# Kernel optimization log

Hardware: AMD Instinct MI355X
Metric: run time of the kernel (lower is better)

The kernel has to match this reference:

```python
import jax, jax.numpy as jnp
import numpy as np

REGION = 64  # region_size r

def setup_inputs() -> dict:
    key = jax.random.key(0)
    B, C, H, W, k, r, T = 16, 64, 256, 256, 3, REGION, 32
    k0, k1, k2, k3, k4 = jax.random.split(key, 5)
    x = jax.random.normal(k0, (B, C, H, W), dtype=jnp.float32)
    weight = jax.random.normal(k1, (C, C, k, k), dtype=jnp.float32) * 0.05  # [out,in,kh,kw]
    h_idx = jax.random.randint(k2, (T,), 0, H - r + 1, dtype=jnp.int32)
    w_idx = jax.random.randint(k3, (T,), 0, W - r + 1, dtype=jnp.int32)
    lambdas = jax.random.uniform(k4, (T,), dtype=jnp.float32)
    return {"x": x, "weight": weight, "h_idx": h_idx, "w_idx": w_idx, "lambdas": lambdas}

def reference(x, weight, h_idx, w_idx, lambdas):
    B, C, H, W = x.shape
    k = weight.shape[-1]
    r = REGION
    n_r = (H // r) * (W // r)
    out_r = r - k + 1  # conv 'VALID' output size per region

    def step(out, t):
        h, w, lam = t
        crop = jax.lax.dynamic_slice(x, (0, 0, h, w), (B, C, r, r))
        c = jax.lax.conv_general_dilated(
            crop, weight, window_strides=(1, 1), padding='VALID',
            dimension_numbers=('NCHW', 'OIHW', 'NCHW'))
        cur = jax.lax.dynamic_slice(out, (0, 0, h, w), (B, C, out_r, out_r))
        out = jax.lax.dynamic_update_slice(out, cur + lam * c, (0, 0, h, w))
        return out, None

    out, _ = jax.lax.scan(step, jnp.zeros_like(x), (h_idx, w_idx, lambdas))
    return out / n_r
```

## Files before the change

kernel.cpp:

```cpp
#include <hip/hip_runtime.h>


typedef short short8 __attribute__((ext_vector_type(8)));
typedef float floatx4 __attribute__((ext_vector_type(4)));
typedef unsigned int uint4v __attribute__((ext_vector_type(4)));

#define OUTR 62

__device__ inline unsigned f2bf_pack(float lo, float hi) {
    unsigned ul = __builtin_bit_cast(unsigned, lo);
    unsigned uh = __builtin_bit_cast(unsigned, hi);
    ul = (ul + 0x7FFFu + ((ul >> 16) & 1u)) >> 16;
    uh = (uh + 0x7FFFu + ((uh >> 16) & 1u)) >> 16;
    return ul | (uh << 16);
}

__global__ void srconv_coeff_kernel(const int* __restrict__ h_idx,
                                    const int* __restrict__ w_idx,
                                    const float* __restrict__ lam,
                                    int T, float* __restrict__ coeff) {
    int p = blockIdx.x;
    int q = threadIdx.x;
    float c = 0.f;
    for (int t = 0; t < T; ++t) {
        int dh = p - h_idx[t];
        int dw = q - w_idx[t];
        if (dh >= 0 && dh < OUTR && dw >= 0 && dw < OUTR) c += lam[t];
    }
    coeff[(p << 8) + q] = c * (1.0f / 16.0f);
}

__global__ void srconv_wtrans_kernel(const float* __restrict__ wgt,
                                     uint4v* __restrict__ afrag) {
    int id = blockIdx.x * 256 + threadIdx.x;
    int l  = id & 63;
    int fi = id >> 6;
    int m  = fi & 3;
    int cb = (fi >> 2) & 1;
    int kk = fi >> 3;
    int co  = m * 16 + (l & 15);
    int ci0 = cb * 32 + (l >> 4) * 8;
    float w[8];
#pragma unroll
    for (int j = 0; j < 8; ++j)
        w[j] = wgt[(co * 64 + ci0 + j) * 9 + kk];
    uint4v d;
    d.x = f2bf_pack(w[0], w[1]);
    d.y = f2bf_pack(w[2], w[3]);
    d.z = f2bf_pack(w[4], w[5]);
    d.w = f2bf_pack(w[6], w[7]);
    afrag[id] = d;
}

__launch_bounds__(256, 2)
__global__ void srconv_fused_kernel(const float* __restrict__ x,
                                    const float* __restrict__ coeff,
                                    const uint4v* __restrict__ afrag,
                                    float* __restrict__ out) {
    __shared__ __align__(16) unsigned xs[2 * 340 * 16];
    __shared__ __align__(16) uint4v af_lds[2304];

    const int tid  = threadIdx.x;
    const int lane = tid & 63;
    const int wv   = tid >> 6;
    const int l15  = lane & 15;
    const int kg   = lane >> 4;

    const unsigned bid = blockIdx.x;
    const unsigned swz = (bid & 7) * 512 + (bid >> 3);
    const int b    = swz >> 8;
    const int tile = swz & 255;
    const int P0   = (tile >> 3) << 3;
    const int Q0   = (tile & 7) << 5;

    float myc = coeff[((P0 + (tid >> 5)) << 8) + Q0 + (tid & 31)];
    if (__syncthreads_count(myc != 0.f) == 0) {
        const floatx4 z = (floatx4){0.f, 0.f, 0.f, 0.f};
        for (int u = tid; u < 64 * 8 * 8; u += 256) {
            int q4 = u & 7;
            int pr = (u >> 3) & 7;
            int co = u >> 6;
            *(floatx4*)(out + (((b << 6) + co) << 16) +
                        ((P0 + pr) << 8) + Q0 + (q4 << 2)) = z;
        }
        return;
    }

    const int prb = P0 + (wv << 1);

    float cf[2][2];
#pragma unroll
    for (int p = 0; p < 2; ++p)
#pragma unroll
        for (int h = 0; h < 2; ++h)
            cf[p][h] = coeff[((prb + p) << 8) + Q0 + (h << 4) + l15];

    const float* xb = x + ((size_t)b << 22);

    floatx4 va[6][2], vb[6][2];
    uint4v  vc[9];

#pragma unroll
    for (int i = 0; i < 9; ++i) {
        int e = i * 256 + tid;
        vc[i] = afrag[e + ((e >> 8) << 8)];
    }
#pragma unroll
    for (int r = 0; r < 6; ++r) {
        int u  = r * 256 + tid;
        int uc = u < 1440 ? u : 1439;
        int cp    = uc / 90;
        int rem   = uc - cp * 90;
        int row   = rem / 9;
        int chunk = rem - row * 9;
        int gr    = min(P0 + row, 255);
        int gcb   = min(Q0 + (chunk << 2), 252);
        const float* xp = xb + (cp << 17) + (gr << 8) + gcb;
        va[r][0] = *(const floatx4*)(xp);
        va[r][1] = *(const floatx4*)(xp + 65536);
    }

#pragma unroll
    for (int i = 0; i < 9; ++i)
        af_lds[i * 256 + tid] = vc[i];
#pragma unroll
    for (int r = 0; r < 6; ++r) {
        int u  = r * 256 + tid;
        int uc = u < 1440 ? u : 1439;
        int cp    = uc / 90;
        int rem   = uc - cp * 90;
        int row   = rem / 9;
        int chunk = rem - row * 9;
        int c4 = chunk << 2;
#pragma unroll
        for (int j = 0; j < 4; ++j) {
            if (u < 1440 && c4 + j < 34) {
                int pix = row * 34 + c4 + j;
                int slot = cp ^ (((pix >> 1) & 3) << 2);
                xs[(pix << 4) + slot] = f2bf_pack(va[r][0][j], va[r][1][j]);
            }
        }
    }

#pragma unroll
    for (int r = 0; r < 6; ++r) {
        int u  = r * 256 + tid;
        int uc = u < 1440 ? u : 1439;
        int cp    = uc / 90;
        int rem   = uc - cp * 90;
        int row   = rem / 9;
        int chunk = rem - row * 9;
        int gr    = min(P0 + row, 255);
        int gcb   = min(Q0 + (chunk << 2), 252);
        const float* xp = xb + ((16 + cp) << 17) + (gr << 8) + gcb;
        vb[r][0] = *(const floatx4*)(xp);
        vb[r][1] = *(const floatx4*)(xp + 65536);
    }
#pragma unroll
    for (int i = 0; i < 9; ++i) {
        int e = i * 256 + tid;
        vc[i] = afrag[e + ((e >> 8) << 8) + 256];
    }
    __syncthreads();

    floatx4 acc[4][2][2];
#pragma unroll
    for (int m = 0; m < 4; ++m)
#pragma unroll
        for (int p = 0; p < 2; ++p)
#pragma unroll
            for (int h = 0; h < 2; ++h)
                acc[m][p][h] = (floatx4){0.f, 0.f, 0.f, 0.f};

#pragma unroll 2
    for (int t = 0; t < 9; ++t) {
        const int kh = t / 3;
        const int kw = t - kh * 3;

        short8 a[4];
#pragma unroll
        for (int m = 0; m < 4; ++m)
            a[m] = *reinterpret_cast<const short8*>(
                &af_lds[(t << 8) + (m << 6) + lane]);
        short8 bf[2][2];
#pragma unroll
        for (int p = 0; p < 2; ++p)
#pragma unroll
            for (int h = 0; h < 2; ++h) {
                int prl = (wv << 1) + p + kh;
                int cl  = (h << 4) + l15 + kw;
                int pix = prl * 34 + cl;
                int off = (pix << 4) +
                          ((kg << 2) ^ (((pix >> 1) & 3) << 2));
                bf[p][h] = *(const short8*)(&xs[off]);
            }
        __builtin_amdgcn_s_setprio(1);
#pragma unroll
        for (int m = 0; m < 4; ++m)
#pragma unroll
            for (int p = 0; p < 2; ++p)
#pragma unroll
                for (int h = 0; h < 2; ++h)
                    acc[m][p][h] = __builtin_amdgcn_mfma_f32_16x16x32_bf16(
                        a[m], bf[p][h], acc[m][p][h], 0, 0, 0);
        __builtin_amdgcn_s_setprio(0);
    }
    __syncthreads();

#pragma unroll
    for (int r = 0; r < 6; ++r) {
        int u  = r * 256 + tid;
        int uc = u < 1440 ? u : 1439;
        int cp    = uc / 90;
        int rem   = uc - cp * 90;
        int row   = rem / 9;
        int chunk = rem - row * 9;
        int c4 = chunk << 2;
#pragma unroll
        for (int j = 0; j < 4; ++j) {
            if (u < 1440 && c4 + j < 34) {
                int pix = row * 34 + c4 + j;
                int slot = cp ^ (((pix >> 1) & 3) << 2);
                xs[5440 + (pix << 4) + slot] =
                    f2bf_pack(vb[r][0][j], vb[r][1][j]);
            }
        }
    }
#pragma unroll
    for (int i = 0; i < 9; ++i)
        af_lds[i * 256 + tid] = vc[i];
    __syncthreads();

#pragma unroll 2
    for (int t = 0; t < 9; ++t) {
        const int kh = t / 3;
        const int kw = t - kh * 3;

        short8 a[4];
#pragma unroll
        for (int m = 0; m < 4; ++m)
            a[m] = *reinterpret_cast<const short8*>(
                &af_lds[(t << 8) + (m << 6) + lane]);
        short8 bf[2][2];
#pragma unroll
        for (int p = 0; p < 2; ++p)
#pragma unroll
            for (int h = 0; h < 2; ++h) {
                int prl = (wv << 1) + p + kh;
                int cl  = (h << 4) + l15 + kw;
                int pix = prl * 34 + cl;
                int off = 5440 + (pix << 4) +
                          ((kg << 2) ^ (((pix >> 1) & 3) << 2));
                bf[p][h] = *(const short8*)(&xs[off]);
            }
        __builtin_amdgcn_s_setprio(1);
#pragma unroll
        for (int m = 0; m < 4; ++m)
#pragma unroll
            for (int p = 0; p < 2; ++p)
#pragma unroll
                for (int h = 0; h < 2; ++h)
                    acc[m][p][h] = __builtin_amdgcn_mfma_f32_16x16x32_bf16(
                        a[m], bf[p][h], acc[m][p][h], 0, 0, 0);
        __builtin_amdgcn_s_setprio(0);
    }
    __syncthreads();

    float* epb = reinterpret_cast<float*>(xs);
    const int co_l = lane >> 3;
    const int q4   = lane & 7;

#pragma unroll
    for (int p = 0; p < 2; ++p) {
        const int pr = prb + p;
#pragma unroll
        for (int m = 0; m < 4; ++m) {
            float* ep = epb + (((wv << 1) + (m & 1)) * 576);
#pragma unroll
            for (int h = 0; h < 2; ++h)
#pragma unroll
                for (int reg = 0; reg < 4; ++reg)
                    ep[((kg << 2) + reg) * 36 + (h << 4) + l15] =
                        acc[m][p][h][reg] * cf[p][h];
#pragma unroll
            for (int j = 0; j < 2; ++j) {
                const floatx4 v = *reinterpret_cast<const floatx4*>(
                    &ep[(co_l + (j << 3)) * 36 + (q4 << 2)]);
                const int co = (m << 4) + co_l + (j << 3);
                *(floatx4*)(out + (((b << 6) + co) << 16) +
                            (pr << 8) + Q0 + (q4 << 2)) = v;
            }
        }
    }
}

extern "C" void kernel_launch(void* const* d_in, const int* in_sizes, int n_in,
                              void* d_out, int out_size, void* d_ws, size_t ws_size,
                              hipStream_t stream) {
    const float* x     = (const float*)d_in[0];
    const float* wgt   = (const float*)d_in[1];
    const int*   h_idx = (const int*)d_in[2];
    const int*   w_idx = (const int*)d_in[3];
    const float* lam   = (const float*)d_in[4];
    float*       out   = (float*)d_out;
    float*       coeff = (float*)d_ws;
    char*        af_b  = (char*)d_ws + 65536 * sizeof(float);
    const int    T     = in_sizes[2];

    srconv_coeff_kernel<<<256, 256, 0, stream>>>(h_idx, w_idx, lam, T, coeff);
    srconv_wtrans_kernel<<<18, 256, 0, stream>>>(wgt, (uint4v*)af_b);
    srconv_fused_kernel<<<4096, 256, 0, stream>>>(
        x, coeff, (const uint4v*)af_b, out);
}
```

Baseline: 169.8 us.

## Process two row-tiles per block with cross-tile prefetch of inputs and weights

Each block now covers 16 output rows as two 8-row sub-tiles, and the grid is halved. Global loads for the next sub-tile's input channels and weight fragments are issued while the current sub-tile is still computing and storing. The epilogue staging moves to the second LDS half so the first half can be refilled early. This aims to hide load latency and amortize per-block setup, at the cost of more register pressure, coarser zero-tile skipping and fewer blocks available for load balancing.

```diff
diff --git a/kernel.cpp b/kernel.cpp
--- a/kernel.cpp
+++ b/kernel.cpp
@@ -67,231 +67,228 @@
     const int kg   = lane >> 4;
 
     const unsigned bid = blockIdx.x;
-    const unsigned swz = (bid & 7) * 512 + (bid >> 3);
-    const int b    = swz >> 8;
-    const int tile = swz & 255;
-    const int P0   = (tile >> 3) << 3;
-    const int Q0   = (tile & 7) << 5;
-
-    float myc = coeff[((P0 + (tid >> 5)) << 8) + Q0 + (tid & 31)];
-    if (__syncthreads_count(myc != 0.f) == 0) {
+    const unsigned swz = (bid & 7) * 256 + (bid >> 3);
+    const int b    = swz >> 7;
+    const int rest = swz & 127;
+    const int R0   = (rest >> 3) << 4;
+    const int Q0   = (rest & 7) << 5;
+
+    float cm = 0.f;
+#pragma unroll
+    for (int i = 0; i < 2; ++i) {
+        int u = i * 256 + tid;
+        cm = fmaxf(cm, coeff[((R0 + (u >> 5)) << 8) + Q0 + (u & 31)]);
+    }
+    if (__syncthreads_count(cm != 0.f) == 0) {
         const floatx4 z = (floatx4){0.f, 0.f, 0.f, 0.f};
-        for (int u = tid; u < 64 * 8 * 8; u += 256) {
+        for (int u = tid; u < 64 * 16 * 8; u += 256) {
             int q4 = u & 7;
-            int pr = (u >> 3) & 7;
-            int co = u >> 6;
+            int pr = (u >> 3) & 15;
+            int co = u >> 7;
             *(floatx4*)(out + (((b << 6) + co) << 16) +
-                        ((P0 + pr) << 8) + Q0 + (q4 << 2)) = z;
+                        ((R0 + pr) << 8) + Q0 + (q4 << 2)) = z;
         }
         return;
     }
-
-    const int prb = P0 + (wv << 1);
-
-    float cf[2][2];
-#pragma unroll
-    for (int p = 0; p < 2; ++p)
-#pragma unroll
-        for (int h = 0; h < 2; ++h)
-            cf[p][h] = coeff[((prb + p) << 8) + Q0 + (h << 4) + l15];
 
     const float* xb = x + ((size_t)b << 22);
 
     floatx4 va[6][2], vb[6][2];
     uint4v  vc[9];
 
-#pragma unroll
-    for (int i = 0; i < 9; ++i) {
-        int e = i * 256 + tid;
-        vc[i] = afrag[e + ((e >> 8) << 8)];
-    }
-#pragma unroll
-    for (int r = 0; r < 6; ++r) {
-        int u  = r * 256 + tid;
-        int uc = u < 1440 ? u : 1439;
-        int cp    = uc / 90;
-        int rem   = uc - cp * 90;
-        int row   = rem / 9;
-        int chunk = rem - row * 9;
-        int gr    = min(P0 + row, 255);
-        int gcb   = min(Q0 + (chunk << 2), 252);
-        const float* xp = xb + (cp << 17) + (gr << 8) + gcb;
-        va[r][0] = *(const floatx4*)(xp);
-        va[r][1] = *(const floatx4*)(xp + 65536);
-    }
-
-#pragma unroll
-    for (int i = 0; i < 9; ++i)
-        af_lds[i * 256 + tid] = vc[i];
-#pragma unroll
-    for (int r = 0; r < 6; ++r) {
-        int u  = r * 256 + tid;
-        int uc = u < 1440 ? u : 1439;
-        int cp    = uc / 90;
-        int rem   = uc - cp * 90;
-        int row   = rem / 9;
-        int chunk = rem - row * 9;
-        int c4 = chunk << 2;
-#pragma unroll
-        for (int j = 0; j < 4; ++j) {
-            if (u < 1440 && c4 + j < 34) {
-                int pix = row * 34 + c4 + j;
-                int slot = cp ^ (((pix >> 1) & 3) << 2);
-                xs[(pix << 4) + slot] = f2bf_pack(va[r][0][j], va[r][1][j]);
-            }
-        }
-    }
-
-#pragma unroll
-    for (int r = 0; r < 6; ++r) {
-        int u  = r * 256 + tid;
-        int uc = u < 1440 ? u : 1439;
-        int cp    = uc / 90;
-        int rem   = uc - cp * 90;
-        int row   = rem / 9;
-        int chunk = rem - row * 9;
-        int gr    = min(P0 + row, 255);
-        int gcb   = min(Q0 + (chunk << 2), 252);
-        const float* xp = xb + ((16 + cp) << 17) + (gr << 8) + gcb;
-        vb[r][0] = *(const floatx4*)(xp);
-        vb[r][1] = *(const floatx4*)(xp + 65536);
-    }
-#pragma unroll
-    for (int i = 0; i < 9; ++i) {
-        int e = i * 256 + tid;
-        vc[i] = afrag[e + ((e >> 8) << 8) + 256];
-    }
+#define ISSUE_A(CB)                                                         \
+    _Pragma("unroll")                                                       \
+    for (int i_ = 0; i_ < 9; ++i_) {                                        \
+        int e_ = i_ * 256 + tid;                                            \
+        vc[i_] = afrag[e_ + ((e_ >> 8) << 8) + ((CB) << 8)];                \
+    }
+#define WRITE_A()                                                           \
+    _Pragma("unroll")                                                       \
+    for (int i_ = 0; i_ < 9; ++i_) af_lds[i_ * 256 + tid] = vc[i_];
+#define ISSUE_X(P0N, CB, V)                                                 \
+    _Pragma("unroll")                                                       \
+    for (int r_ = 0; r_ < 6; ++r_) {                                        \
+        int u_  = r_ * 256 + tid;                                           \
+        int uc_ = u_ < 1440 ? u_ : 1439;                                    \
+        int cp_    = uc_ / 90;                                              \
+        int rem_   = uc_ - cp_ * 90;                                        \
+        int row_   = rem_ / 9;                                              \
+        int chunk_ = rem_ - row_ * 9;                                       \
+        int gr_    = min((P0N) + row_, 255);                                \
+        int gcb_   = min(Q0 + (chunk_ << 2), 252);                          \
+        const float* xp_ = xb + ((((CB) << 4) + cp_) << 17) +               \
+                           (gr_ << 8) + gcb_;                               \
+        V[r_][0] = *(const floatx4*)(xp_);                                  \
+        V[r_][1] = *(const floatx4*)(xp_ + 65536);                          \
+    }
+#define WRITE_X(OFF, V)                                                     \
+    _Pragma("unroll")                                                       \
+    for (int r_ = 0; r_ < 6; ++r_) {                                        \
+        int u_  = r_ * 256 + tid;                                           \
+        int uc_ = u_ < 1440 ? u_ : 1439;                                    \
+        int cp_    = uc_ / 90;                                              \
+        int rem_   = uc_ - cp_ * 90;                                        \
+        int row_   = rem_ / 9;                                              \
+        int chunk_ = rem_ - row_ * 9;                                       \
+        int c4_ = chunk_ << 2;                                              \
+        _Pragma("unroll")                                                   \
+        for (int j_ = 0; j_ < 4; ++j_) {                                    \
+            if (u_ < 1440 && c4_ + j_ < 34) {                               \
+                int pix_  = row_ * 34 + c4_ + j_;                           \
+                int slot_ = cp_ ^ (((pix_ >> 1) & 3) << 2);                 \
+                xs[(OFF) + (pix_ << 4) + slot_] =                           \
+                    f2bf_pack(V[r_][0][j_], V[r_][1][j_]);                  \
+            }                                                               \
+        }                                                                   \
+    }
+
+    ISSUE_A(0);
+    ISSUE_X(R0, 0, va);
+    WRITE_A();
+    WRITE_X(0, va);
+    ISSUE_X(R0, 1, vb);
+    ISSUE_A(1);
     __syncthreads();
 
-    floatx4 acc[4][2][2];
-#pragma unroll
-    for (int m = 0; m < 4; ++m)
-#pragma unroll
-        for (int p = 0; p < 2; ++p)
-#pragma unroll
-            for (int h = 0; h < 2; ++h)
-                acc[m][p][h] = (floatx4){0.f, 0.f, 0.f, 0.f};
-
-#pragma unroll 2
-    for (int t = 0; t < 9; ++t) {
-        const int kh = t / 3;
-        const int kw = t - kh * 3;
-
-        short8 a[4];
-#pragma unroll
-        for (int m = 0; m < 4; ++m)
-            a[m] = *reinterpret_cast<const short8*>(
-                &af_lds[(t << 8) + (m << 6) + lane]);
-        short8 bf[2][2];
-#pragma unroll
-        for (int p = 0; p < 2; ++p)
-#pragma unroll
-            for (int h = 0; h < 2; ++h) {
-                int prl = (wv << 1) + p + kh;
-                int cl  = (h << 4) + l15 + kw;
-                int pix = prl * 34 + cl;
-                int off = (pix << 4) +
-                          ((kg << 2) ^ (((pix >> 1) & 3) << 2));
-                bf[p][h] = *(const short8*)(&xs[off]);
-            }
-        __builtin_amdgcn_s_setprio(1);
-#pragma unroll
-        for (int m = 0; m < 4; ++m)
-#pragma unroll
-            for (int p = 0; p < 2; ++p)
-#pragma unroll
-                for (int h = 0; h < 2; ++h)
-                    acc[m][p][h] = __builtin_amdgcn_mfma_f32_16x16x32_bf16(
-                        a[m], bf[p][h], acc[m][p][h], 0, 0, 0);
-        __builtin_amdgcn_s_setprio(0);
-    }
-    __syncthreads();
-
-#pragma unroll
-    for (int r = 0; r < 6; ++r) {
-        int u  = r * 256 + tid;
-        int uc = u < 1440 ? u : 1439;
-        int cp    = uc / 90;
-        int rem   = uc - cp * 90;
-        int row   = rem / 9;
-        int chunk = rem - row * 9;
-        int c4 = chunk << 2;
-#pragma unroll
-        for (int j = 0; j < 4; ++j) {
-            if (u < 1440 && c4 + j < 34) {
-                int pix = row * 34 + c4 + j;
-                int slot = cp ^ (((pix >> 1) & 3) << 2);
-                xs[5440 + (pix << 4) + slot] =
-                    f2bf_pack(vb[r][0][j], vb[r][1][j]);
-            }
-        }
-    }
-#pragma unroll
-    for (int i = 0; i < 9; ++i)
-        af_lds[i * 256 + tid] = vc[i];
-    __syncthreads();
-
-#pragma unroll 2
-    for (int t = 0; t < 9; ++t) {
-        const int kh = t / 3;
-        const int kw = t - kh * 3;
-
-        short8 a[4];
-#pragma unroll
-        for (int m = 0; m < 4; ++m)
-            a[m] = *reinterpret_cast<const short8*>(
-                &af_lds[(t << 8) + (m << 6) + lane]);
-        short8 bf[2][2];
-#pragma unroll
-        for (int p = 0; p < 2; ++p)
-#pragma unroll
-            for (int h = 0; h < 2; ++h) {
-                int prl = (wv << 1) + p + kh;
-                int cl  = (h << 4) + l15 + kw;
-                int pix = prl * 34 + cl;
-                int off = 5440 + (pix << 4) +
-                          ((kg << 2) ^ (((pix >> 1) & 3) << 2));
-                bf[p][h] = *(const short8*)(&xs[off]);
-            }
-        __builtin_amdgcn_s_setprio(1);
-#pragma unroll
-        for (int m = 0; m < 4; ++m)
-#pragma unroll
-            for (int p = 0; p < 2; ++p)
-#pragma unroll
-                for (int h = 0; h < 2; ++h)
-                    acc[m][p][h] = __builtin_amdgcn_mfma_f32_16x16x32_bf16(
-                        a[m], bf[p][h], acc[m][p][h], 0, 0, 0);
-        __builtin_amdgcn_s_setprio(0);
-    }
-    __syncthreads();
-
-    float* epb = reinterpret_cast<float*>(xs);
     const int co_l = lane >> 3;
     const int q4   = lane & 7;
 
 #pragma unroll
-    for (int p = 0; p < 2; ++p) {
-        const int pr = prb + p;
-#pragma unroll
-        for (int m = 0; m < 4; ++m) {
-            float* ep = epb + (((wv << 1) + (m & 1)) * 576);
+    for (int s = 0; s < 2; ++s) {
+        const int P0  = R0 + (s << 3);
+        const int prb = P0 + (wv << 1);
+
+        float cf[2][2];
+#pragma unroll
+        for (int p = 0; p < 2; ++p)
 #pragma unroll
             for (int h = 0; h < 2; ++h)
-#pragma unroll
-                for (int reg = 0; reg < 4; ++reg)
-                    ep[((kg << 2) + reg) * 36 + (h << 4) + l15] =
-                        acc[m][p][h][reg] * cf[p][h];
-#pragma unroll
-            for (int j = 0; j < 2; ++j) {
-                const floatx4 v = *reinterpret_cast<const floatx4*>(
-                    &ep[(co_l + (j << 3)) * 36 + (q4 << 2)]);
-                const int co = (m << 4) + co_l + (j << 3);
-                *(floatx4*)(out + (((b << 6) + co) << 16) +
-                            (pr << 8) + Q0 + (q4 << 2)) = v;
+                cf[p][h] = coeff[((prb + p) << 8) + Q0 + (h << 4) + l15];
+
+        floatx4 acc[4][2][2];
+#pragma unroll
+        for (int m = 0; m < 4; ++m)
+#pragma unroll
+            for (int p = 0; p < 2; ++p)
+#pragma unroll
+                for (int h = 0; h < 2; ++h)
+                    acc[m][p][h] = (floatx4){0.f, 0.f, 0.f, 0.f};
+
+#pragma unroll 2
+        for (int t = 0; t < 9; ++t) {
+            const int kh = t / 3;
+            const int kw = t - kh * 3;
+            short8 a[4];
+#pragma unroll
+            for (int m = 0; m < 4; ++m)
+                a[m] = *reinterpret_cast<const short8*>(
+                    &af_lds[(t << 8) + (m << 6) + lane]);
+            short8 bf[2][2];
+#pragma unroll
+            for (int p = 0; p < 2; ++p)
+#pragma unroll
+                for (int h = 0; h < 2; ++h) {
+                    int prl = (wv << 1) + p + kh;
+                    int cl  = (h << 4) + l15 + kw;
+                    int pix = prl * 34 + cl;
+                    int off = (pix << 4) +
+                              ((kg << 2) ^ (((pix >> 1) & 3) << 2));
+                    bf[p][h] = *(const short8*)(&xs[off]);
+                }
+            __builtin_amdgcn_s_setprio(1);
+#pragma unroll
+            for (int m = 0; m < 4; ++m)
+#pragma unroll
+                for (int p = 0; p < 2; ++p)
+#pragma unroll
+                    for (int h = 0; h < 2; ++h)
+                        acc[m][p][h] = __builtin_amdgcn_mfma_f32_16x16x32_bf16(
+                            a[m], bf[p][h], acc[m][p][h], 0, 0, 0);
+            __builtin_amdgcn_s_setprio(0);
+        }
+        __syncthreads();
+
+        WRITE_X(5440, vb);
+        WRITE_A();
+        if (s == 0) {
+            ISSUE_X(R0 + 8, 0, va);
+            ISSUE_A(0);
+        }
+        __syncthreads();
+
+#pragma unroll 2
+        for (int t = 0; t < 9; ++t) {
+            const int kh = t / 3;
+            const int kw = t - kh * 3;
+            short8 a[4];
+#pragma unroll
+            for (int m = 0; m < 4; ++m)
+                a[m] = *reinterpret_cast<const short8*>(
+                    &af_lds[(t << 8) + (m << 6) + lane]);
+            short8 bf[2][2];
+#pragma unroll
+            for (int p = 0; p < 2; ++p)
+#pragma unroll
+                for (int h = 0; h < 2; ++h) {
+                    int prl = (wv << 1) + p + kh;
+                    int cl  = (h << 4) + l15 + kw;
+                    int pix = prl * 34 + cl;
+                    int off = 5440 + (pix << 4) +
+                              ((kg << 2) ^ (((pix >> 1) & 3) << 2));
+                    bf[p][h] = *(const short8*)(&xs[off]);
+                }
+            __builtin_amdgcn_s_setprio(1);
+#pragma unroll
+            for (int m = 0; m < 4; ++m)
+#pragma unroll
+                for (int p = 0; p < 2; ++p)
+#pragma unroll
+                    for (int h = 0; h < 2; ++h)
+                        acc[m][p][h] = __builtin_amdgcn_mfma_f32_16x16x32_bf16(
+                            a[m], bf[p][h], acc[m][p][h], 0, 0, 0);
+            __builtin_amdgcn_s_setprio(0);
+        }
+        __syncthreads();
+
+        if (s == 0) {
+            WRITE_X(0, va);
+            WRITE_A();
+        }
+
+        float* epb = reinterpret_cast<float*>(xs) + 5440;
+#pragma unroll
+        for (int p = 0; p < 2; ++p) {
+            const int pr = prb + p;
+#pragma unroll
+            for (int m = 0; m < 4; ++m) {
+                float* ep = epb + (((wv << 1) + (m & 1)) * 576);
+#pragma unroll
+                for (int h = 0; h < 2; ++h)
+#pragma unroll
+                    for (int reg = 0; reg < 4; ++reg)
+                        ep[((kg << 2) + reg) * 36 + (h << 4) + l15] =
+                            acc[m][p][h][reg] * cf[p][h];
+#pragma unroll
+                for (int j = 0; j < 2; ++j) {
+                    const floatx4 v = *reinterpret_cast<const floatx4*>(
+                        &ep[(co_l + (j << 3)) * 36 + (q4 << 2)]);
+                    const int co = (m << 4) + co_l + (j << 3);
+                    *(floatx4*)(out + (((b << 6) + co) << 16) +
+                                (pr << 8) + Q0 + (q4 << 2)) = v;
+                }
             }
         }
-    }
+
+        if (s == 0) {
+            ISSUE_X(R0 + 8, 1, vb);
+            ISSUE_A(1);
+            __syncthreads();
+        }
+    }
+#undef ISSUE_A
+#undef WRITE_A
+#undef ISSUE_X
+#undef WRITE_X
 }
 
 extern "C" void kernel_launch(void* const* d_in, const int* in_sizes, int n_in,
@@ -309,6 +306,6 @@
 
     srconv_coeff_kernel<<<256, 256, 0, stream>>>(h_idx, w_idx, lam, T, coeff);
     srconv_wtrans_kernel<<<18, 256, 0, stream>>>(wgt, (uint4v*)af_b);
-    srconv_fused_kernel<<<4096, 256, 0, stream>>>(
+    srconv_fused_kernel<<<2048, 256, 0, stream>>>(
         x, coeff, (const uint4v*)af_b, out);
 }
```

Result: slower. 262.3 us (+54.5%).
